# Performance work log

Measured on AMD Instinct MI355X. Metric: run time of the kernel, lower is better.

Reference implementation:

```python
import jax, jax.numpy as jnp
import numpy as np
import math

B, N, K, C_IN, C_OUT = 2, 16384, 16, 128, 128


def _gather_neighbors(x, idx):
    # x: [B, N, C], idx: [B, N, K] -> [B, N, K, C]
    return jax.vmap(lambda xb, ib: xb[ib])(x, idx)


def setup_inputs() -> dict:
    key = jax.random.key(0)
    k1, k2, k3 = jax.random.split(key, 3)
    x = jax.random.normal(k1, (B, N, C_IN), dtype=jnp.float32)
    edge_index = jax.random.randint(k2, (2, B, N, K), 0, N, dtype=jnp.int64)
    W = jax.random.normal(k3, (C_OUT, C_IN), dtype=jnp.float32) * (1.0 / math.sqrt(C_IN))
    b = jnp.zeros((C_OUT,), dtype=jnp.float32)
    return {"x": x, "edge_index": edge_index, "W": W, "b": b}


def reference(x, edge_index, W, b):
    # x: [B, N, C]; edge_index: [2, B, N, K]
    x_i = _gather_neighbors(x, edge_index[1])  # [B, N, K, C] (centers)
    x_j = _gather_neighbors(x, edge_index[0])  # [B, N, K, C] (neighbors)
    scale = 1.0 / math.sqrt(x_i.shape[-1])
    scores = jnp.einsum('bnkc,bnjc->bnkj', x_i, x_j) * scale  # [B, N, K, K]
    p_attn = jax.nn.softmax(scores, axis=-1)
    h_k = jnp.einsum('bnkj,bnjc->bnkc', p_attn, x_j).sum(axis=-2)  # [B, N, C]
    y = (x + h_k) @ W.T + b  # Linear(in_channels -> out_channels)
    return jax.nn.relu(y)
```

## Files before the change

kernel.cpp:

```cpp
#include <hip/hip_runtime.h>
#include <hip/hip_bf16.h>
#include <math.h>

#define BB 2
#define NN 16384
#define KK 16
#define CC 128
#define COUT 128
#define NODES (BB * NN)
#define SP 136
#define SQP 136
#define ZP 136
#define XBLK 2048

typedef __attribute__((ext_vector_type(8))) short bf16x8;
typedef __attribute__((ext_vector_type(4))) float f32x4;
typedef __attribute__((ext_vector_type(2))) float f32x2;

__device__ __forceinline__ bf16x8 cvt8(f32x4 a, f32x4 b) {
    union { bf16x8 v; __hip_bfloat162 h[4]; } u;
    u.h[0] = __float22bfloat162_rn(make_float2(a[0], a[1]));
    u.h[1] = __float22bfloat162_rn(make_float2(a[2], a[3]));
    u.h[2] = __float22bfloat162_rn(make_float2(b[0], b[1]));
    u.h[3] = __float22bfloat162_rn(make_float2(b[2], b[3]));
    return u.v;
}

template <int CTRL>
__device__ __forceinline__ float rot_add(float v) {
    int r = __builtin_amdgcn_update_dpp(0, __float_as_int(v), CTRL, 0xF, 0xF, true);
    return v + __int_as_float(r);
}
__device__ __forceinline__ float row16_sum(float v) {
    v = rot_add<0x128>(v); v = rot_add<0x124>(v);
    v = rot_add<0x122>(v); v = rot_add<0x121>(v);
    return v;
}
__device__ __forceinline__ float row16_sum4(float v) {
    v = rot_add<0x128>(v); v = rot_add<0x124>(v);
    return v;
}

__global__ __launch_bounds__(256) void cast_x(
    const float* __restrict__ x,
    __hip_bfloat16* __restrict__ xh,
    unsigned char* __restrict__ xq,
    const float* __restrict__ W,
    __hip_bfloat16* __restrict__ wh)
{
    const int bid = blockIdx.x;
    if (bid >= XBLK) {
        const int i = (bid - XBLK) * 256 + threadIdx.x;
        const f32x4* p = (const f32x4*)(W + (size_t)i * 8);
        f32x4 a = p[0];
        f32x4 b = p[1];
        *(bf16x8*)(wh + (size_t)i * 8) = cvt8(a, b);
        return;
    }
    const int i = bid * 256 + threadIdx.x;
    const f32x4* p = (const f32x4*)(x + (size_t)i * 8);
    f32x4 a = __builtin_nontemporal_load(p);
    f32x4 b = __builtin_nontemporal_load(p + 1);
    *(bf16x8*)(xh + (size_t)i * 8) = cvt8(a, b);
    int lo = __builtin_amdgcn_cvt_pk_fp8_f32(a[0], a[1], 0, false);
    lo     = __builtin_amdgcn_cvt_pk_fp8_f32(a[2], a[3], lo, true);
    int hi = __builtin_amdgcn_cvt_pk_fp8_f32(b[0], b[1], 0, false);
    hi     = __builtin_amdgcn_cvt_pk_fp8_f32(b[2], b[3], hi, true);
    int2 v; v.x = lo; v.y = hi;
    *(int2*)(xq + (size_t)i * 8) = v;
}

__device__ __forceinline__ float col_weight(f32x4 acc) {
    const float scale = 0.08838834764831843f;
    float w = 0.f;
    #pragma unroll
    for (int i = 0; i < 4; ++i) {
        float e = __expf(acc[i] * scale);
        float s = row16_sum(e);
        w += e * __builtin_amdgcn_rcpf(s);
    }
    w += __shfl_xor(w, 16, 64);
    w += __shfl_xor(w, 32, 64);
    return w;
}

__device__ __forceinline__ float2 reduce_h(const bf16x8* bfr, float wj,
                                           float* hb, int m, int q, int lane) {
    #pragma unroll
    for (int s = 0; s < 4; ++s) {
        union { bf16x8 v; unsigned short u[8]; } ub;
        ub.v = bfr[s];
        float f[8];
        #pragma unroll
        for (int e = 0; e < 8; ++e) {
            f[e] = __uint_as_float((unsigned)ub.u[e] << 16) * wj;
            f[e] = row16_sum4(f[e]);
        }
        if (m < 4) {
            f32x4 lo = {f[0], f[1], f[2], f[3]};
            f32x4 hi = {f[4], f[5], f[6], f[7]};
            *(f32x4*)&hb[m * 132 + 32 * s + 8 * q]     = lo;
            *(f32x4*)&hb[m * 132 + 32 * s + 8 * q + 4] = hi;
        }
    }
    float hx = 0.f, hy = 0.f;
    #pragma unroll
    for (int r = 0; r < 4; ++r) {
        float2 v = *(const float2*)&hb[r * 132 + 2 * lane];
        hx += v.x; hy += v.y;
    }
    return make_float2(hx, hy);
}

struct Gath { int2 q[4]; bf16x8 j[4]; __hip_bfloat162 rx; };

__device__ __forceinline__ void gather_node(
    int node, int r, int c, int lane,
    const __hip_bfloat16* __restrict__ xh,
    const unsigned char* __restrict__ xq,
    const int* __restrict__ edge,
    Gath& g)
{
    const int b = node >> 14;
    const __hip_bfloat16* xbh = xh + (size_t)b * (size_t)(NN * CC);
    const unsigned char*  xbq = xq + (size_t)b * (size_t)(NN * CC);
    const int* ej = edge + (size_t)node * KK;
    const int* ei = ej + (size_t)NODES * KK;
    #pragma unroll
    for (int gg = 0; gg < 4; ++gg) {
        int ridx = __builtin_nontemporal_load(ei + gg * 4 + r);
        g.q[gg] = *(const int2*)(xbq + (size_t)ridx * CC + c * 8);
    }
    #pragma unroll
    for (int gg = 0; gg < 4; ++gg) {
        int ridx = __builtin_nontemporal_load(ej + gg * 4 + r);
        g.j[gg] = *(const bf16x8*)(xbh + (size_t)ridx * CC + c * 8);
    }
    const int n0 = node & (NN - 1);
    g.rx = *(const __hip_bfloat162*)(xbh + (size_t)n0 * CC + 2 * lane);
}

__global__ __launch_bounds__(256, 4) void attn_fused(
    const __hip_bfloat16* __restrict__ xh,
    const unsigned char* __restrict__ xq,
    const int* __restrict__ edge,
    const __hip_bfloat16* __restrict__ wh,
    const float* __restrict__ bias,
    float* __restrict__ out)
{
    __shared__ __hip_bfloat16 stgj[4][16 * SP];
    __shared__ alignas(16) unsigned char stgq[4][16 * SQP];
    __shared__ alignas(16) float hbuf[4][544];
    __shared__ __hip_bfloat16 zt[16][ZP];

    const int t = threadIdx.x;
    const int wv = t >> 6;
    const int lane = t & 63;
    const int m = lane & 15;
    const int q = lane >> 4;
    const int r = lane >> 4;
    const int c = lane & 15;
    const int base = blockIdx.x * 16;

    __hip_bfloat16* sj = &stgj[wv][0];
    unsigned char*  sq = &stgq[wv][0];

    Gath cur, nxt;
    gather_node(base + wv * 4, r, c, lane, xh, xq, edge, cur);

    #pragma unroll
    for (int it = 0; it < 4; ++it) {
        #pragma unroll
        for (int g = 0; g < 4; ++g)
            *(int2*)(sq + (g * 4 + r) * SQP + c * 8) = cur.q[g];
        #pragma unroll
        for (int g = 0; g < 4; ++g)
            *(bf16x8*)(sj + (g * 4 + r) * SP + c * 8) = cur.j[g];

        if (it < 3)
            gather_node(base + wv * 4 + it + 1, r, c, lane, xh, xq, edge, nxt);

        bf16x8 afr[4], bfr[4];
        #pragma unroll
        for (int s = 0; s < 4; ++s) {
            int2 wb = *(const int2*)(sq + m * SQP + s * 32 + q * 8);
            f32x2 f0 = __builtin_amdgcn_cvt_pk_f32_fp8(wb.x, false);
            f32x2 f1 = __builtin_amdgcn_cvt_pk_f32_fp8(wb.x, true);
            f32x2 f2 = __builtin_amdgcn_cvt_pk_f32_fp8(wb.y, false);
            f32x2 f3 = __builtin_amdgcn_cvt_pk_f32_fp8(wb.y, true);
            union { bf16x8 v; __hip_bfloat162 h[4]; } u;
            u.h[0] = __float22bfloat162_rn(make_float2(f0[0], f0[1]));
            u.h[1] = __float22bfloat162_rn(make_float2(f1[0], f1[1]));
            u.h[2] = __float22bfloat162_rn(make_float2(f2[0], f2[1]));
            u.h[3] = __float22bfloat162_rn(make_float2(f3[0], f3[1]));
            afr[s] = u.v;
            bfr[s] = *(const bf16x8*)(sj + m * SP + s * 32 + q * 8);
        }

        f32x4 acc = {0.f, 0.f, 0.f, 0.f};
        #pragma unroll
        for (int s = 0; s < 4; ++s)
            acc = __builtin_amdgcn_mfma_f32_16x16x32_bf16(afr[s], bfr[s], acc, 0, 0, 0);

        const float wj = col_weight(acc);
        float2 h = reduce_h(bfr, wj, &hbuf[wv][0], m, q, lane);

        float2 xc = __bfloat1622float2(cur.rx);
        const int row = wv * 4 + it;
        *(__hip_bfloat162*)(&zt[row][2 * lane]) =
            __float22bfloat162_rn(make_float2(xc.x + h.x, xc.y + h.y));

        if (it < 3) cur = nxt;
    }

    __syncthreads();

    bf16x8 zfr[4];
    #pragma unroll
    for (int s = 0; s < 4; ++s)
        zfr[s] = *(const bf16x8*)(&zt[m][s * 32 + q * 8]);

    #pragma unroll
    for (int half = 0; half < 2; ++half) {
        const int ct = wv * 2 + half;
        const __hip_bfloat16* wp = wh + (size_t)(ct * 16 + m) * CC + q * 8;
        bf16x8 wfr[4];
        #pragma unroll
        for (int s = 0; s < 4; ++s)
            wfr[s] = *(const bf16x8*)(wp + s * 32);
        const float bv = bias[ct * 16 + m];
        f32x4 acc = {0.f, 0.f, 0.f, 0.f};
        #pragma unroll
        for (int s = 0; s < 4; ++s)
            acc = __builtin_amdgcn_mfma_f32_16x16x32_bf16(zfr[s], wfr[s], acc, 0, 0, 0);
        float* op = out + (size_t)(base + q * 4) * COUT + ct * 16 + m;
        #pragma unroll
        for (int i = 0; i < 4; ++i)
            op[(size_t)i * COUT] = fmaxf(acc[i] + bv, 0.f);
    }
}

extern "C" void kernel_launch(void* const* d_in, const int* in_sizes, int n_in,
                              void* d_out, int out_size, void* d_ws, size_t ws_size,
                              hipStream_t stream) {
    const float* x    = (const float*)d_in[0];
    const int*   edge = (const int*)d_in[1];
    const float* W    = (const float*)d_in[2];
    const float* bias = (const float*)d_in[3];
    float* out = (float*)d_out;
    __hip_bfloat16* xh = (__hip_bfloat16*)d_ws;
    unsigned char*  xq = (unsigned char*)d_ws + 8 * 1024 * 1024;
    __hip_bfloat16* wh = (__hip_bfloat16*)((char*)d_ws + 12 * 1024 * 1024);

    cast_x<<<XBLK + (COUT * CC) / (256 * 8), 256, 0, stream>>>(x, xh, xq, W, wh);
    attn_fused<<<NODES / 16, 256, 0, stream>>>(xh, xq, edge, wh, bias, out);
}
```

Measured before the change: 107.7 us.

## Preload edge indices via shuffles, alias reduction buffer on staging LDS, raise occupancy

Each wave now loads the edge indices for all four of its nodes up front, one index per lane, and hands them out to the gathering lanes with shuffles. This replaces per-gather redundant index loads. The center-row loads for all four nodes are also hoisted. The separate hbuf LDS buffer is removed and the reduction scratch is aliased onto the fp8 staging buffer, which cuts shared memory per block, and launch bounds go from 4 to 5 blocks per SM. The fp8 conversion is interleaved with the MFMA chain. The trade-off is more live registers for the preloaded indices and rows, which may conflict with the higher occupancy target.

```diff
diff --git a/kernel.cpp b/kernel.cpp
--- a/kernel.cpp
+++ b/kernel.cpp
@@ -112,35 +112,27 @@
     return make_float2(hx, hy);
 }
 
-struct Gath { int2 q[4]; bf16x8 j[4]; __hip_bfloat162 rx; };
-
-__device__ __forceinline__ void gather_node(
-    int node, int r, int c, int lane,
-    const __hip_bfloat16* __restrict__ xh,
-    const unsigned char* __restrict__ xq,
-    const int* __restrict__ edge,
-    Gath& g)
+struct Rows { int2 q[4]; bf16x8 j[4]; };
+
+__device__ __forceinline__ void gather_rows(
+    int ejv, int eiv, int r, int c,
+    const __hip_bfloat16* __restrict__ xbh,
+    const unsigned char* __restrict__ xbq,
+    Rows& g)
 {
-    const int b = node >> 14;
-    const __hip_bfloat16* xbh = xh + (size_t)b * (size_t)(NN * CC);
-    const unsigned char*  xbq = xq + (size_t)b * (size_t)(NN * CC);
-    const int* ej = edge + (size_t)node * KK;
-    const int* ei = ej + (size_t)NODES * KK;
     #pragma unroll
     for (int gg = 0; gg < 4; ++gg) {
-        int ridx = __builtin_nontemporal_load(ei + gg * 4 + r);
-        g.q[gg] = *(const int2*)(xbq + (size_t)ridx * CC + c * 8);
+        int ri = __shfl(eiv, gg * 4 + r, 16);
+        g.q[gg] = *(const int2*)(xbq + (size_t)ri * CC + c * 8);
     }
     #pragma unroll
     for (int gg = 0; gg < 4; ++gg) {
-        int ridx = __builtin_nontemporal_load(ej + gg * 4 + r);
-        g.j[gg] = *(const bf16x8*)(xbh + (size_t)ridx * CC + c * 8);
-    }
-    const int n0 = node & (NN - 1);
-    g.rx = *(const __hip_bfloat162*)(xbh + (size_t)n0 * CC + 2 * lane);
-}
-
-__global__ __launch_bounds__(256, 4) void attn_fused(
+        int rj = __shfl(ejv, gg * 4 + r, 16);
+        g.j[gg] = *(const bf16x8*)(xbh + (size_t)rj * CC + c * 8);
+    }
+}
+
+__global__ __launch_bounds__(256, 5) void attn_fused(
     const __hip_bfloat16* __restrict__ xh,
     const unsigned char* __restrict__ xq,
     const int* __restrict__ edge,
@@ -150,7 +142,6 @@
 {
     __shared__ __hip_bfloat16 stgj[4][16 * SP];
     __shared__ alignas(16) unsigned char stgq[4][16 * SQP];
-    __shared__ alignas(16) float hbuf[4][544];
     __shared__ __hip_bfloat16 zt[16][ZP];
 
     const int t = threadIdx.x;
@@ -161,12 +152,28 @@
     const int r = lane >> 4;
     const int c = lane & 15;
     const int base = blockIdx.x * 16;
-
+    const int node0 = base + wv * 4;
+    const int b = node0 >> 14;
+
+    const __hip_bfloat16* xbh = xh + (size_t)b * (size_t)(NN * CC);
+    const unsigned char*  xbq = xq + (size_t)b * (size_t)(NN * CC);
     __hip_bfloat16* sj = &stgj[wv][0];
     unsigned char*  sq = &stgq[wv][0];
-
-    Gath cur, nxt;
-    gather_node(base + wv * 4, r, c, lane, xh, xq, edge, cur);
+    float*          hb = (float*)sq;
+
+    int ejv[4], eiv[4];
+    __hip_bfloat162 rxv[4];
+    #pragma unroll
+    for (int n = 0; n < 4; ++n) {
+        const int* ej = edge + (size_t)(node0 + n) * KK;
+        ejv[n] = __builtin_nontemporal_load(ej + m);
+        eiv[n] = __builtin_nontemporal_load(ej + (size_t)NODES * KK + m);
+        const int nloc = (node0 + n) & (NN - 1);
+        rxv[n] = *(const __hip_bfloat162*)(xbh + (size_t)nloc * CC + 2 * lane);
+    }
+
+    Rows cur, nxt;
+    gather_rows(ejv[0], eiv[0], r, c, xbh, xbq, cur);
 
     #pragma unroll
     for (int it = 0; it < 4; ++it) {
@@ -178,12 +185,14 @@
             *(bf16x8*)(sj + (g * 4 + r) * SP + c * 8) = cur.j[g];
 
         if (it < 3)
-            gather_node(base + wv * 4 + it + 1, r, c, lane, xh, xq, edge, nxt);
-
-        bf16x8 afr[4], bfr[4];
+            gather_rows(ejv[it + 1], eiv[it + 1], r, c, xbh, xbq, nxt);
+
+        bf16x8 bfr[4];
+        f32x4 acc = {0.f, 0.f, 0.f, 0.f};
         #pragma unroll
         for (int s = 0; s < 4; ++s) {
             int2 wb = *(const int2*)(sq + m * SQP + s * 32 + q * 8);
+            bfr[s] = *(const bf16x8*)(sj + m * SP + s * 32 + q * 8);
             f32x2 f0 = __builtin_amdgcn_cvt_pk_f32_fp8(wb.x, false);
             f32x2 f1 = __builtin_amdgcn_cvt_pk_f32_fp8(wb.x, true);
             f32x2 f2 = __builtin_amdgcn_cvt_pk_f32_fp8(wb.y, false);
@@ -193,19 +202,13 @@
             u.h[1] = __float22bfloat162_rn(make_float2(f1[0], f1[1]));
             u.h[2] = __float22bfloat162_rn(make_float2(f2[0], f2[1]));
             u.h[3] = __float22bfloat162_rn(make_float2(f3[0], f3[1]));
-            afr[s] = u.v;
-            bfr[s] = *(const bf16x8*)(sj + m * SP + s * 32 + q * 8);
+            acc = __builtin_amdgcn_mfma_f32_16x16x32_bf16(u.v, bfr[s], acc, 0, 0, 0);
         }
 
-        f32x4 acc = {0.f, 0.f, 0.f, 0.f};
-        #pragma unroll
-        for (int s = 0; s < 4; ++s)
-            acc = __builtin_amdgcn_mfma_f32_16x16x32_bf16(afr[s], bfr[s], acc, 0, 0, 0);
-
         const float wj = col_weight(acc);
-        float2 h = reduce_h(bfr, wj, &hbuf[wv][0], m, q, lane);
-
-        float2 xc = __bfloat1622float2(cur.rx);
+        float2 h = reduce_h(bfr, wj, hb, m, q, lane);
+
+        float2 xc = __bfloat1622float2(rxv[it]);
         const int row = wv * 4 + it;
         *(__hip_bfloat162*)(&zt[row][2 * lane]) =
             __float22bfloat162_rn(make_float2(xc.x + h.x, xc.y + h.y));
```

Measured after the change: 108.1 us. No clear change (+0.4%).
